# Optimization experiments

Hardware: AMD Instinct MI355X
Metric: run time of the kernel (lower is better)

## Reference

```python
import jax, jax.numpy as jnp
import numpy as np

N_NODES = 50000
N_EDGES = 1600000
FEAT = 1536
HID = 200
NCLS = 2


def setup_inputs() -> dict:
    key = jax.random.key(0)
    ks = jax.random.split(key, 12)
    x = jax.random.normal(ks[0], (N_NODES, FEAT), dtype=jnp.float32)
    edge_src = jax.random.randint(ks[1], (N_EDGES,), 0, N_NODES, dtype=jnp.int32)
    edge_dst = jax.random.randint(ks[2], (N_EDGES,), 0, N_NODES, dtype=jnp.int32)
    edge_w = jax.random.uniform(ks[3], (N_EDGES,), dtype=jnp.float32)
    s1 = 1.0 / np.sqrt(768.0)
    s2 = 1.0 / np.sqrt(HID)
    return {
        "x": x,
        "edge_src": edge_src,
        "edge_dst": edge_dst,
        "edge_w": edge_w,
        "W1a": jax.random.normal(ks[4], (768, HID), dtype=jnp.float32) * s1,
        "b1a": jnp.zeros((HID,), jnp.float32),
        "W2a": jax.random.normal(ks[5], (HID, NCLS), dtype=jnp.float32) * s2,
        "b2a": jnp.zeros((NCLS,), jnp.float32),
        "W1b": jax.random.normal(ks[6], (768, HID), dtype=jnp.float32) * s1,
        "b1b": jnp.zeros((HID,), jnp.float32),
        "W2b": jax.random.normal(ks[7], (HID, NCLS), dtype=jnp.float32) * s2,
        "b2b": jnp.zeros((NCLS,), jnp.float32),
    }


def _gcn_conv(x, W, b, src, dst, w, activation):
    # GCNConv: activation(A @ (X @ W) + b) with sparse A given as edge list
    h = x @ W                                  # [N, out] dense transform first (out < in)
    msg = h[src] * w[:, None]                  # [E, out] weighted messages
    agg = jax.ops.segment_sum(msg, dst, num_segments=x.shape[0])  # [N, out]
    return activation(agg + b)


def reference(x, edge_src, edge_dst, edge_w, W1a, b1a, W2a, b2a, W1b, b1b, W2b, b2b):
    x1 = x[:, :768]
    x2 = x[:, 768:]
    # Expert 1 branch (dropout is identity at inference)
    h1 = _gcn_conv(x1, W1a, b1a, edge_src, edge_dst, edge_w, jax.nn.relu)
    p1 = _gcn_conv(h1, W2a, b2a, edge_src, edge_dst, edge_w,
                   lambda z: jax.nn.softmax(z, axis=-1))
    # Expert 2 branch
    h2 = _gcn_conv(x2, W1b, b1b, edge_src, edge_dst, edge_w, jax.nn.relu)
    p2 = _gcn_conv(h2, W2b, b2b, edge_src, edge_dst, edge_w,
                   lambda z: jax.nn.softmax(z, axis=-1))
    # Inference-mode soft voting: elementwise max then renormalize
    votes = jnp.maximum(p1, p2)
    votes = votes / jnp.sum(votes, axis=1, keepdims=True)
    return votes
```

## Files before the change

### kernel.cpp

```cpp
#include <hip/hip_runtime.h>
#include <hip/hip_fp16.h>

#define N_NODES 50000
#define N_EDGES 1600000
#define FEAT    1536
#define HID     200
#define HIDP    208
#define HID2    416
#define KDIM    768
#define CAP     96

typedef _Float16 half8 __attribute__((ext_vector_type(8)));
typedef _Float16 half4 __attribute__((ext_vector_type(4)));
typedef float   float4v __attribute__((ext_vector_type(4)));

__global__ void prep_kernel(const float* __restrict__ W1a, const float* __restrict__ b1a,
                            const float* __restrict__ W2a,
                            const float* __restrict__ W1b, const float* __restrict__ b1b,
                            const float* __restrict__ W2b,
                            _Float16* __restrict__ Wht, float* __restrict__ b1comb,
                            float* __restrict__ W2comb) {
  int i = blockIdx.x * 256 + threadIdx.x;
  if (i < 2 * HIDP * KDIM) {
    int br = i / (HIDP * KDIM);
    int r  = i % (HIDP * KDIM);
    int n = r / KDIM, k = r % KDIM;
    const float* W = br ? W1b : W1a;
    Wht[i] = (n < HID) ? (_Float16)W[k * HID + n] : (_Float16)0.0f;
  }
  if (i < HID2) {
    int br = i / HIDP, c = i % HIDP;
    const float* b  = br ? b1b : b1a;
    const float* W2 = br ? W2b : W2a;
    bool ok = (c < HID);
    b1comb[i]       = ok ? b[c]        : 0.0f;
    W2comb[2*i + 0] = ok ? W2[c*2 + 0] : 0.0f;
    W2comb[2*i + 1] = ok ? W2[c*2 + 1] : 0.0f;
  }
}

__global__ void append_kernel(const int* __restrict__ src, const int* __restrict__ dst,
                              const float* __restrict__ w, int* __restrict__ cnt,
                              int2* __restrict__ ssw) {
  int i = blockIdx.x * 256 + threadIdx.x;
  if (i < N_EDGES) {
    int d = dst[i];
    int pos = atomicAdd(&cnt[d], 1);
    if (pos < CAP)
      ssw[(size_t)d * CAP + pos] = make_int2(src[i], __float_as_int(w[i]));
  }
}

__global__ __launch_bounds__(256, 2) void gemm1_kernel(const float* __restrict__ x,
    const _Float16* __restrict__ Wht, _Float16* __restrict__ hpre) {
  const int m0 = blockIdx.x * 128;
  const int br = blockIdx.y;
  const int tid = threadIdx.x;
  const int wave = tid >> 6, lane = tid & 63;
  __shared__ _Float16 Alds[128][40];
  __shared__ _Float16 Blds[HIDP][40];
  const _Float16* Wb = Wht + (size_t)br * HIDP * KDIM;
  float4v acc[2][13];
#pragma unroll
  for (int mt = 0; mt < 2; ++mt)
#pragma unroll
    for (int nt = 0; nt < 13; ++nt) acc[mt][nt] = (float4v){0.f, 0.f, 0.f, 0.f};

  const int mlo = lane & 15, kq = (lane >> 4) * 8;

  for (int k0 = 0; k0 < KDIM; k0 += 32) {
    __syncthreads();
#pragma unroll
    for (int p = 0; p < 4; ++p) {
      int idx = tid + p * 256;
      int row = idx >> 3, c4 = idx & 7;
      int grow = m0 + row; if (grow > N_NODES - 1) grow = N_NODES - 1;
      const float4v xv = __builtin_nontemporal_load(
          (const float4v*)(x + (size_t)grow * FEAT + br * KDIM + k0 + c4 * 4));
      half4 hv = {(_Float16)xv[0], (_Float16)xv[1], (_Float16)xv[2], (_Float16)xv[3]};
      *(half4*)&Alds[row][c4 * 4] = hv;
    }
    for (int idx = tid; idx < HIDP * 4; idx += 256) {
      int n = idx >> 2, c = idx & 3;
      *(half8*)&Blds[n][c * 8] = *(const half8*)(Wb + n * KDIM + k0 + c * 8);
    }
    __syncthreads();
    half8 a0 = *(half8*)&Alds[wave * 32 + mlo][kq];
    half8 a1 = *(half8*)&Alds[wave * 32 + 16 + mlo][kq];
#pragma unroll
    for (int nt = 0; nt < 13; ++nt) {
      half8 b = *(half8*)&Blds[nt * 16 + mlo][kq];
      acc[0][nt] = __builtin_amdgcn_mfma_f32_16x16x32_f16(a0, b, acc[0][nt], 0, 0, 0);
      acc[1][nt] = __builtin_amdgcn_mfma_f32_16x16x32_f16(a1, b, acc[1][nt], 0, 0, 0);
    }
  }
  const int nlo = lane & 15, mq = (lane >> 4) * 4;
#pragma unroll
  for (int mt = 0; mt < 2; ++mt)
#pragma unroll
    for (int nt = 0; nt < 13; ++nt)
#pragma unroll
      for (int r = 0; r < 4; ++r) {
        int row = m0 + wave * 32 + mt * 16 + mq + r;
        if (row < N_NODES)
          hpre[(size_t)row * HID2 + br * HIDP + nt * 16 + nlo] = (_Float16)acc[mt][nt][r];
      }
}

__global__ __launch_bounds__(256) void agg1_kernel(const int2* __restrict__ ssw,
    const int* __restrict__ cnt, const _Float16* __restrict__ hpre,
    const float* __restrict__ b1comb, const float* __restrict__ W2comb,
    float4v* __restrict__ qtab) {
  const int d = blockIdx.x * 4 + (threadIdx.x >> 6);
  const int lane = threadIdx.x & 63;
  const bool actA = (lane < 26);
  const bool actB = (lane >= 32 && lane < 58);
  const bool act  = actA || actB;
  const int col = actA ? lane * 8 : (actB ? 208 + (lane - 32) * 8 : 0);
  const int e0 = d * CAP;
  const int deg = min(cnt[d], CAP);
  const int e1 = e0 + deg;
  float acc[8];
#pragma unroll
  for (int j = 0; j < 8; ++j) acc[j] = 0.f;
  if (act) {
    const _Float16* hp = hpre + col;
    int e = e0;
    for (; e + 3 < e1; e += 4) {
      int2 s0 = ssw[e], s1 = ssw[e + 1], s2 = ssw[e + 2], s3 = ssw[e + 3];
      half8 h0 = *(const half8*)(hp + (size_t)s0.x * HID2);
      half8 h1 = *(const half8*)(hp + (size_t)s1.x * HID2);
      half8 h2 = *(const half8*)(hp + (size_t)s2.x * HID2);
      half8 h3 = *(const half8*)(hp + (size_t)s3.x * HID2);
      float w0 = __int_as_float(s0.y), w1 = __int_as_float(s1.y);
      float w2 = __int_as_float(s2.y), w3 = __int_as_float(s3.y);
#pragma unroll
      for (int j = 0; j < 8; ++j)
        acc[j] += w0 * (float)h0[j] + w1 * (float)h1[j]
                + w2 * (float)h2[j] + w3 * (float)h3[j];
    }
    for (; e < e1; ++e) {
      int2 s0 = ssw[e];
      half8 h0 = *(const half8*)(hp + (size_t)s0.x * HID2);
      float w0 = __int_as_float(s0.y);
#pragma unroll
      for (int j = 0; j < 8; ++j) acc[j] += w0 * (float)h0[j];
    }
  }
  float p0 = 0.f, p1 = 0.f;
  if (act) {
#pragma unroll
    for (int j = 0; j < 8; ++j) {
      int c = col + j;
      float h = fmaxf(acc[j] + b1comb[c], 0.f);
      p0 += h * W2comb[2 * c + 0];
      p1 += h * W2comb[2 * c + 1];
    }
  }
#pragma unroll
  for (int off = 16; off > 0; off >>= 1) {
    p0 += __shfl_xor(p0, off);
    p1 += __shfl_xor(p1, off);
  }
  float q2 = __shfl(p0, 32);
  float q3 = __shfl(p1, 32);
  if (lane == 0) qtab[d] = (float4v){p0, p1, q2, q3};
}

__global__ __launch_bounds__(256) void agg2_kernel(const int2* __restrict__ ssw,
    const int* __restrict__ cnt, const float4v* __restrict__ qtab,
    const float* __restrict__ b2a, const float* __restrict__ b2b,
    float* __restrict__ out) {
  const int d = blockIdx.x * 8 + (threadIdx.x >> 5);
  const int lane = threadIdx.x & 31;
  const int e0 = d * CAP;
  const int e1 = e0 + min(cnt[d], CAP);
  float a0 = 0.f, a1 = 0.f, a2 = 0.f, a3 = 0.f;
  for (int e = e0 + lane; e < e1; e += 32) {
    int2 sw = ssw[e];
    float w = __int_as_float(sw.y);
    float4v q = qtab[sw.x];
    a0 += w * q[0]; a1 += w * q[1]; a2 += w * q[2]; a3 += w * q[3];
  }
#pragma unroll
  for (int off = 16; off > 0; off >>= 1) {
    a0 += __shfl_xor(a0, off);
    a1 += __shfl_xor(a1, off);
    a2 += __shfl_xor(a2, off);
    a3 += __shfl_xor(a3, off);
  }
  if (lane == 0) {
    float za0 = a0 + b2a[0], za1 = a1 + b2a[1];
    float zb0 = a2 + b2b[0], zb1 = a3 + b2b[1];
    float m1 = fmaxf(za0, za1);
    float ea0 = __expf(za0 - m1), ea1 = __expf(za1 - m1);
    float p10 = ea0 / (ea0 + ea1), p11 = ea1 / (ea0 + ea1);
    float m2 = fmaxf(zb0, zb1);
    float eb0 = __expf(zb0 - m2), eb1 = __expf(zb1 - m2);
    float p20 = eb0 / (eb0 + eb1), p21 = eb1 / (eb0 + eb1);
    float v0 = fmaxf(p10, p20), v1 = fmaxf(p11, p21);
    float s = v0 + v1;
    out[d * 2 + 0] = v0 / s;
    out[d * 2 + 1] = v1 / s;
  }
}

extern "C" void kernel_launch(void* const* d_in, const int* in_sizes, int n_in,
                              void* d_out, int out_size, void* d_ws, size_t ws_size,
                              hipStream_t stream) {
  const float* x        = (const float*)d_in[0];
  const int*   edge_src = (const int*)d_in[1];
  const int*   edge_dst = (const int*)d_in[2];
  const float* edge_w   = (const float*)d_in[3];
  const float* W1a = (const float*)d_in[4];
  const float* b1a = (const float*)d_in[5];
  const float* W2a = (const float*)d_in[6];
  const float* b2a = (const float*)d_in[7];
  const float* W1b = (const float*)d_in[8];
  const float* b1b = (const float*)d_in[9];
  const float* W2b = (const float*)d_in[10];
  const float* b2b = (const float*)d_in[11];
  float* out = (float*)d_out;

  char* ws = (char*)d_ws;
  size_t off = 0;
  auto alloc = [&](size_t bytes) -> void* {
    void* p = ws + off;
    off = (off + bytes + 255) & ~(size_t)255;
    return p;
  };
  _Float16* Wht  = (_Float16*)alloc((size_t)2 * HIDP * KDIM * sizeof(_Float16));
  float* b1comb  = (float*)alloc(HID2 * sizeof(float));
  float* W2comb  = (float*)alloc(HID2 * 2 * sizeof(float));
  int* cnt       = (int*)alloc(N_NODES * sizeof(int));
  int2* ssw      = (int2*)alloc((size_t)N_NODES * CAP * sizeof(int2));
  float4v* qtab  = (float4v*)alloc((size_t)N_NODES * sizeof(float4v));
  _Float16* hpre = (_Float16*)alloc((size_t)N_NODES * HID2 * sizeof(_Float16));
  (void)ws_size; (void)in_sizes; (void)n_in; (void)out_size;

  (void)hipMemsetAsync(cnt, 0, N_NODES * sizeof(int), stream);

  prep_kernel<<<dim3((2 * HIDP * KDIM + 255) / 256), dim3(256), 0, stream>>>(
      W1a, b1a, W2a, W1b, b1b, W2b, Wht, b1comb, W2comb);
  append_kernel<<<dim3((N_EDGES + 255) / 256), dim3(256), 0, stream>>>(
      edge_src, edge_dst, edge_w, cnt, ssw);
  gemm1_kernel<<<dim3((N_NODES + 127) / 128, 2), dim3(256), 0, stream>>>(x, Wht, hpre);
  agg1_kernel<<<dim3(N_NODES / 4), dim3(256), 0, stream>>>(ssw, cnt, hpre, b1comb, W2comb, qtab);
  agg2_kernel<<<dim3(N_NODES / 8), dim3(256), 0, stream>>>(ssw, cnt, qtab, b2a, b2b, out);
}
```

Baseline: 780.8 us.

## Fuse edge append and first GEMM into one launch; compact hidden layout

```diff
diff --git a/kernel.cpp b/kernel.cpp
--- a/kernel.cpp
+++ b/kernel.cpp
@@ -6,9 +6,10 @@
 #define FEAT    1536
 #define HID     200
 #define HIDP    208
-#define HID2    416
+#define HPW     400
 #define KDIM    768
 #define CAP     96
+#define NAPP    2048
 
 typedef _Float16 half8 __attribute__((ext_vector_type(8)));
 typedef _Float16 half4 __attribute__((ext_vector_type(4)));
@@ -28,37 +29,40 @@
     const float* W = br ? W1b : W1a;
     Wht[i] = (n < HID) ? (_Float16)W[k * HID + n] : (_Float16)0.0f;
   }
-  if (i < HID2) {
-    int br = i / HIDP, c = i % HIDP;
+  if (i < 2 * HID) {
+    int br = i / HID, cc = i % HID;
     const float* b  = br ? b1b : b1a;
     const float* W2 = br ? W2b : W2a;
-    bool ok = (c < HID);
-    b1comb[i]       = ok ? b[c]        : 0.0f;
-    W2comb[2*i + 0] = ok ? W2[c*2 + 0] : 0.0f;
-    W2comb[2*i + 1] = ok ? W2[c*2 + 1] : 0.0f;
-  }
-}
-
-__global__ void append_kernel(const int* __restrict__ src, const int* __restrict__ dst,
-                              const float* __restrict__ w, int* __restrict__ cnt,
-                              int2* __restrict__ ssw) {
-  int i = blockIdx.x * 256 + threadIdx.x;
-  if (i < N_EDGES) {
-    int d = dst[i];
-    int pos = atomicAdd(&cnt[d], 1);
-    if (pos < CAP)
-      ssw[(size_t)d * CAP + pos] = make_int2(src[i], __float_as_int(w[i]));
-  }
-}
-
-__global__ __launch_bounds__(256, 2) void gemm1_kernel(const float* __restrict__ x,
-    const _Float16* __restrict__ Wht, _Float16* __restrict__ hpre) {
-  const int m0 = blockIdx.x * 128;
-  const int br = blockIdx.y;
-  const int tid = threadIdx.x;
-  const int wave = tid >> 6, lane = tid & 63;
+    b1comb[i]       = b[cc];
+    W2comb[2*i + 0] = W2[cc*2 + 0];
+    W2comb[2*i + 1] = W2[cc*2 + 1];
+  }
+}
+
+__global__ __launch_bounds__(256, 2) void fused_kernel(
+    const int* __restrict__ esrc, const int* __restrict__ edst,
+    const float* __restrict__ ew, int* __restrict__ cnt, int2* __restrict__ ssw,
+    const float* __restrict__ x, const _Float16* __restrict__ Wht,
+    _Float16* __restrict__ hpre) {
   __shared__ _Float16 Alds[128][40];
   __shared__ _Float16 Blds[HIDP][40];
+  const int bid = blockIdx.x;
+  const int tid = threadIdx.x;
+
+  if (bid < NAPP) {
+    for (int i = bid * 256 + tid; i < N_EDGES; i += NAPP * 256) {
+      int d = edst[i];
+      int pos = atomicAdd(&cnt[d], 1);
+      if (pos < CAP)
+        ssw[(size_t)d * CAP + pos] = make_int2(esrc[i], __float_as_int(ew[i]));
+    }
+    return;
+  }
+
+  const int gid = bid - NAPP;
+  const int m0 = (gid >> 1) * 128;
+  const int br = gid & 1;
+  const int wave = tid >> 6, lane = tid & 63;
   const _Float16* Wb = Wht + (size_t)br * HIDP * KDIM;
   float4v acc[2][13];
 #pragma unroll
@@ -98,13 +102,16 @@
 #pragma unroll
   for (int mt = 0; mt < 2; ++mt)
 #pragma unroll
-    for (int nt = 0; nt < 13; ++nt)
-#pragma unroll
-      for (int r = 0; r < 4; ++r) {
-        int row = m0 + wave * 32 + mt * 16 + mq + r;
-        if (row < N_NODES)
-          hpre[(size_t)row * HID2 + br * HIDP + nt * 16 + nlo] = (_Float16)acc[mt][nt][r];
-      }
+    for (int nt = 0; nt < 13; ++nt) {
+      int c = nt * 16 + nlo;
+      if (c < HID)
+#pragma unroll
+        for (int r = 0; r < 4; ++r) {
+          int row = m0 + wave * 32 + mt * 16 + mq + r;
+          if (row < N_NODES)
+            hpre[(size_t)row * HPW + br * HID + c] = (_Float16)acc[mt][nt][r];
+        }
+    }
 }
 
 __global__ __launch_bounds__(256) void agg1_kernel(const int2* __restrict__ ssw,
@@ -113,10 +120,10 @@
     float4v* __restrict__ qtab) {
   const int d = blockIdx.x * 4 + (threadIdx.x >> 6);
   const int lane = threadIdx.x & 63;
-  const bool actA = (lane < 26);
-  const bool actB = (lane >= 32 && lane < 58);
+  const bool actA = (lane < 25);
+  const bool actB = (lane >= 32 && lane < 57);
   const bool act  = actA || actB;
-  const int col = actA ? lane * 8 : (actB ? 208 + (lane - 32) * 8 : 0);
+  const int col = actA ? lane * 8 : (actB ? HID + (lane - 32) * 8 : 0);
   const int e0 = d * CAP;
   const int deg = min(cnt[d], CAP);
   const int e1 = e0 + deg;
@@ -128,10 +135,10 @@
     int e = e0;
     for (; e + 3 < e1; e += 4) {
       int2 s0 = ssw[e], s1 = ssw[e + 1], s2 = ssw[e + 2], s3 = ssw[e + 3];
-      half8 h0 = *(const half8*)(hp + (size_t)s0.x * HID2);
-      half8 h1 = *(const half8*)(hp + (size_t)s1.x * HID2);
-      half8 h2 = *(const half8*)(hp + (size_t)s2.x * HID2);
-      half8 h3 = *(const half8*)(hp + (size_t)s3.x * HID2);
+      half8 h0 = *(const half8*)(hp + (size_t)s0.x * HPW);
+      half8 h1 = *(const half8*)(hp + (size_t)s1.x * HPW);
+      half8 h2 = *(const half8*)(hp + (size_t)s2.x * HPW);
+      half8 h3 = *(const half8*)(hp + (size_t)s3.x * HPW);
       float w0 = __int_as_float(s0.y), w1 = __int_as_float(s1.y);
       float w2 = __int_as_float(s2.y), w3 = __int_as_float(s3.y);
 #pragma unroll
@@ -141,7 +148,7 @@
     }
     for (; e < e1; ++e) {
       int2 s0 = ssw[e];
-      half8 h0 = *(const half8*)(hp + (size_t)s0.x * HID2);
+      half8 h0 = *(const half8*)(hp + (size_t)s0.x * HPW);
       float w0 = __int_as_float(s0.y);
 #pragma unroll
       for (int j = 0; j < 8; ++j) acc[j] += w0 * (float)h0[j];
@@ -230,21 +237,20 @@
     return p;
   };
   _Float16* Wht  = (_Float16*)alloc((size_t)2 * HIDP * KDIM * sizeof(_Float16));
-  float* b1comb  = (float*)alloc(HID2 * sizeof(float));
-  float* W2comb  = (float*)alloc(HID2 * 2 * sizeof(float));
+  float* b1comb  = (float*)alloc(2 * HID * sizeof(float));
+  float* W2comb  = (float*)alloc(2 * HID * 2 * sizeof(float));
   int* cnt       = (int*)alloc(N_NODES * sizeof(int));
   int2* ssw      = (int2*)alloc((size_t)N_NODES * CAP * sizeof(int2));
   float4v* qtab  = (float4v*)alloc((size_t)N_NODES * sizeof(float4v));
-  _Float16* hpre = (_Float16*)alloc((size_t)N_NODES * HID2 * sizeof(_Float16));
+  _Float16* hpre = (_Float16*)alloc((size_t)N_NODES * HPW * sizeof(_Float16));
   (void)ws_size; (void)in_sizes; (void)n_in; (void)out_size;
 
   (void)hipMemsetAsync(cnt, 0, N_NODES * sizeof(int), stream);
 
   prep_kernel<<<dim3((2 * HIDP * KDIM + 255) / 256), dim3(256), 0, stream>>>(
       W1a, b1a, W2a, W1b, b1b, W2b, Wht, b1comb, W2comb);
-  append_kernel<<<dim3((N_EDGES + 255) / 256), dim3(256), 0, stream>>>(
-      edge_src, edge_dst, edge_w, cnt, ssw);
-  gemm1_kernel<<<dim3((N_NODES + 127) / 128, 2), dim3(256), 0, stream>>>(x, Wht, hpre);
+  fused_kernel<<<dim3(NAPP + ((N_NODES + 127) / 128) * 2), dim3(256), 0, stream>>>(
+      edge_src, edge_dst, edge_w, cnt, ssw, x, Wht, hpre);
   agg1_kernel<<<dim3(N_NODES / 4), dim3(256), 0, stream>>>(ssw, cnt, hpre, b1comb, W2comb, qtab);
   agg2_kernel<<<dim3(N_NODES / 8), dim3(256), 0, stream>>>(ssw, cnt, qtab, b2a, b2b, out);
 }
```

Measured after the change: 772.7 us. Within noise of the previous version (-1.0%).
